# Performance work log

Hardware: AMD Instinct MI355X
Metric: run time of the kernel (lower is better)

The kernel has to match this reference:

```python
import jax, jax.numpy as jnp
import numpy as np

B, T, D, W, H = 4096, 1, 4096, 4, 512  # batch, step len, hidden, kernel_size, generator hidden


def setup_inputs() -> dict:
    key = jax.random.key(0)
    ks = jax.random.split(key, 5)
    x = jax.random.normal(ks[0], (B, T, D), dtype=jnp.float32)
    generator_input = jax.random.normal(ks[1], (B, T, D), dtype=jnp.float32)
    cache = jax.random.normal(ks[2], (B, D, W), dtype=jnp.float32)
    w1 = jax.random.normal(ks[3], (D, H), dtype=jnp.float32) * 0.02
    w2 = jax.random.normal(ks[4], (H, D * W), dtype=jnp.float32) * 0.02
    b2 = jnp.zeros((D * W,), dtype=jnp.float32)
    return {"x": x, "generator_input": generator_input, "cache": cache,
            "w1": w1, "w2": w2, "b2": b2}


def reference(x, generator_input, cache, w1, w2, b2):
    # --- kernel generator (DynamicShortConvolutionKernelGenerator) ---
    g = generator_input[:, 0]                        # [B, D]  (squeeze(1) in _step_triton)
    h = jax.nn.silu(g @ w1)                          # [B, H]
    flat_kernels = h @ w2 + b2                       # [B, D*W]
    kernels = flat_kernels.reshape(B, D, W)          # [B, D, W]  (rearrange 'b (d w) -> b d w')
    # --- causal_conv_step_triton: shift window left, append new token ---
    x_t = jnp.swapaxes(x, 1, 2)                      # [B, D, 1]
    new_cache = jnp.concatenate([cache[:, :, 1:], x_t], axis=-1)  # [B, D, W]
    # depthwise dynamic conv: per-token, per-channel kernel dot window
    out = jnp.sum(new_cache * kernels, axis=-1)      # [B, D]
    out = jax.nn.silu(out)[:, None, :]               # [B, 1, D] (view back to x shape)
    return out, new_cache
```

## Files before the change

kernel.cpp:

```cpp
#include <hip/hip_runtime.h>
#include <hip/hip_bf16.h>
#include <math.h>

#define B_  4096
#define D_  4096
#define W_  4
#define H_  512
#define NDW (D_*W_)

typedef float  f32x4  __attribute__((ext_vector_type(4)));
typedef __bf16 bf16x8 __attribute__((ext_vector_type(8)));

__device__ __forceinline__ unsigned short f32_to_bf16(float f) {
    unsigned int u = __float_as_uint(f);
    u += 0x7fffu + ((u >> 16) & 1u);
    return (unsigned short)(u >> 16);
}

__device__ __forceinline__ float silu_f(float v) {
    return v / (1.0f + __expf(-v));
}

__global__ void cast_g_kernel(const float* __restrict__ in,
                              unsigned short* __restrict__ out, int n4) {
    int i = blockIdx.x * blockDim.x + threadIdx.x;
    if (i >= n4) return;
    float4 v = ((const float4*)in)[i];
    ushort4 o;
    o.x = f32_to_bf16(v.x); o.y = f32_to_bf16(v.y);
    o.z = f32_to_bf16(v.z); o.w = f32_to_bf16(v.w);
    ((ushort4*)out)[i] = o;
}

__global__ void transpose_cast_kernel(const float* __restrict__ in,
                                      unsigned short* __restrict__ out,
                                      int R, int C) {
    __shared__ unsigned short tile[64][65];
    const int r0 = blockIdx.y * 64;
    const int c0 = blockIdx.x * 64;
    const int tx = threadIdx.x & 63;
    const int ty = threadIdx.x >> 6;
#pragma unroll
    for (int rr = ty; rr < 64; rr += 4)
        tile[rr][tx] = f32_to_bf16(in[(size_t)(r0 + rr) * C + c0 + tx]);
    __syncthreads();
#pragma unroll
    for (int cc = ty; cc < 64; cc += 4)
        out[(size_t)(c0 + cc) * R + r0 + tx] = tile[tx][cc];
}

template<int EPI>
__global__ __launch_bounds__(256)
void gemm_bt(const unsigned short* __restrict__ A,
             const unsigned short* __restrict__ Bt,
             unsigned short* __restrict__ Hout,
             float* __restrict__ Fout,
             const float* __restrict__ bias,
             int M, int N, int K)
{
    __shared__ unsigned short As[128 * 64];
    __shared__ unsigned short Bs[128 * 64];

    const int tid  = threadIdx.x;
    const int wave = tid >> 6;
    const int lane = tid & 63;
    const int quad = lane >> 4;
    const int l16  = lane & 15;
    const int m0 = blockIdx.y * 128;
    const int n0 = blockIdx.x * 128;
    const int wm = (wave >> 1) * 64;
    const int wn = (wave & 1) * 64;

    f32x4 acc[4][4];
#pragma unroll
    for (int i = 0; i < 4; ++i)
#pragma unroll
        for (int j = 0; j < 4; ++j)
            acc[i][j] = (f32x4){0.f, 0.f, 0.f, 0.f};

    for (int k0 = 0; k0 < K; k0 += 64) {
#pragma unroll
        for (int r = 0; r < 4; ++r) {
            const int flat  = r * 256 + tid;
            const int row   = flat >> 3;
            const int chunk = flat & 7;
            const unsigned short* gA = A  + (size_t)(m0 + row) * K + (k0 + chunk * 8);
            const unsigned short* gB = Bt + (size_t)(n0 + row) * K + (k0 + chunk * 8);
            unsigned short* lA = As + (size_t)(r * 256 + wave * 64) * 8;
            unsigned short* lB = Bs + (size_t)(r * 256 + wave * 64) * 8;
            __builtin_amdgcn_global_load_lds(
                (const __attribute__((address_space(1))) void*)gA,
                (__attribute__((address_space(3))) void*)lA, 16, 0, 0);
            __builtin_amdgcn_global_load_lds(
                (const __attribute__((address_space(1))) void*)gB,
                (__attribute__((address_space(3))) void*)lB, 16, 0, 0);
        }
        __syncthreads();

#pragma unroll
        for (int ks = 0; ks < 2; ++ks) {
            const int kk = ks * 32 + quad * 8;
            bf16x8 af[4], bfr[4];
#pragma unroll
            for (int i = 0; i < 4; ++i) {
                af[i]  = *(const bf16x8*)(As + (wm + i * 16 + l16) * 64 + kk);
                bfr[i] = *(const bf16x8*)(Bs + (wn + i * 16 + l16) * 64 + kk);
            }
#pragma unroll
            for (int i = 0; i < 4; ++i)
#pragma unroll
                for (int j = 0; j < 4; ++j)
                    acc[i][j] = __builtin_amdgcn_mfma_f32_16x16x32_bf16(
                        af[i], bfr[j], acc[i][j], 0, 0, 0);
        }
        __syncthreads();
    }

#pragma unroll
    for (int i = 0; i < 4; ++i) {
#pragma unroll
        for (int j = 0; j < 4; ++j) {
            const int col = n0 + wn + j * 16 + l16;
#pragma unroll
            for (int r = 0; r < 4; ++r) {
                const int row = m0 + wm + i * 16 + quad * 4 + r;
                float v = acc[i][j][r];
                if (EPI == 0) {
                    Hout[(size_t)row * N + col] = f32_to_bf16(silu_f(v));
                } else {
                    Fout[(size_t)row * N + col] = v + bias[col];
                }
            }
        }
    }
}

__global__ void conv_kernel(const float* __restrict__ x,
                            const float* __restrict__ cache,
                            float* __restrict__ out,
                            float* __restrict__ kc, int n) {
    int i = blockIdx.x * blockDim.x + threadIdx.x;
    if (i >= n) return;
    float4 k4 = ((const float4*)kc)[i];
    float4 c4 = ((const float4*)cache)[i];
    float  xv = x[i];
    float4 nc;
    nc.x = c4.y; nc.y = c4.z; nc.z = c4.w; nc.w = xv;
    float s = nc.x * k4.x + nc.y * k4.y + nc.z * k4.z + nc.w * k4.w;
    out[i] = silu_f(s);
    ((float4*)kc)[i] = nc;
}

extern "C" void kernel_launch(void* const* d_in, const int* in_sizes, int n_in,
                              void* d_out, int out_size, void* d_ws, size_t ws_size,
                              hipStream_t stream) {
    const float* x     = (const float*)d_in[0];
    const float* gin   = (const float*)d_in[1];
    const float* cache = (const float*)d_in[2];
    const float* w1    = (const float*)d_in[3];
    const float* w2    = (const float*)d_in[4];
    const float* b2    = (const float*)d_in[5];

    float* out    = (float*)d_out;
    float* ncache = out + (size_t)B_ * D_;

    unsigned short* g_bf = (unsigned short*)d_ws;
    unsigned short* w1t  = g_bf + (size_t)B_ * D_;
    unsigned short* w2t  = w1t + (size_t)H_ * D_;
    unsigned short* h_bf = w2t + (size_t)NDW * H_;

    cast_g_kernel<<<(B_ * D_ / 4 + 255) / 256, 256, 0, stream>>>(gin, g_bf, B_ * D_ / 4);
    transpose_cast_kernel<<<dim3(H_ / 64, D_ / 64), 256, 0, stream>>>(w1, w1t, D_, H_);
    transpose_cast_kernel<<<dim3(NDW / 64, H_ / 64), 256, 0, stream>>>(w2, w2t, H_, NDW);

    gemm_bt<0><<<dim3(H_ / 128, B_ / 128), 256, 0, stream>>>(
        g_bf, w1t, h_bf, nullptr, nullptr, B_, H_, D_);

    gemm_bt<1><<<dim3(NDW / 128, B_ / 128), 256, 0, stream>>>(
        h_bf, w2t, nullptr, ncache, b2, B_, NDW, H_);

    conv_kernel<<<(B_ * D_ + 255) / 256, 256, 0, stream>>>(x, cache, out, ncache, B_ * D_);
}
```

Measured before the change: 854.6 us.

## Fuse depthwise conv into second GEMM epilogue and shrink first GEMM M-tile

The second GEMM no longer writes the full B x D*W fp32 kernel tensor to global memory for a separate conv kernel to read back. It stages each half of its output tile in shared memory, adds the bias, and computes the shifted cache window, dot product, SiLU and new-cache write in place. The first GEMM now uses 64-row M tiles, doubling block count from 128 to 256 to fill more compute units. The cost is extra shared-memory staging, two additional barriers per block, and a longer epilogue.

```diff
diff --git a/kernel.cpp b/kernel.cpp
--- a/kernel.cpp
+++ b/kernel.cpp
@@ -49,17 +49,103 @@
         out[(size_t)(c0 + cc) * R + r0 + tx] = tile[tx][cc];
 }
 
-template<int EPI>
 __global__ __launch_bounds__(256)
-void gemm_bt(const unsigned short* __restrict__ A,
-             const unsigned short* __restrict__ Bt,
-             unsigned short* __restrict__ Hout,
-             float* __restrict__ Fout,
-             const float* __restrict__ bias,
-             int M, int N, int K)
+void gemm1_silu(const unsigned short* __restrict__ A,
+                const unsigned short* __restrict__ Bt,
+                unsigned short* __restrict__ Hout,
+                int M, int N, int K)
 {
-    __shared__ unsigned short As[128 * 64];
+    __shared__ unsigned short As[64 * 64];
     __shared__ unsigned short Bs[128 * 64];
+
+    const int tid  = threadIdx.x;
+    const int wave = tid >> 6;
+    const int lane = tid & 63;
+    const int quad = lane >> 4;
+    const int l16  = lane & 15;
+    const int m0 = blockIdx.y * 64;
+    const int n0 = blockIdx.x * 128;
+    const int wm = (wave >> 1) * 32;
+    const int wn = (wave & 1) * 64;
+
+    f32x4 acc[2][4];
+#pragma unroll
+    for (int i = 0; i < 2; ++i)
+#pragma unroll
+        for (int j = 0; j < 4; ++j)
+            acc[i][j] = (f32x4){0.f, 0.f, 0.f, 0.f};
+
+    for (int k0 = 0; k0 < K; k0 += 64) {
+#pragma unroll
+        for (int r = 0; r < 2; ++r) {
+            const int flat  = r * 256 + tid;
+            const int row   = flat >> 3;
+            const int chunk = flat & 7;
+            const unsigned short* gA = A + (size_t)(m0 + row) * K + (k0 + chunk * 8);
+            unsigned short* lA = As + (size_t)(r * 256 + wave * 64) * 8;
+            __builtin_amdgcn_global_load_lds(
+                (const __attribute__((address_space(1))) void*)gA,
+                (__attribute__((address_space(3))) void*)lA, 16, 0, 0);
+        }
+#pragma unroll
+        for (int r = 0; r < 4; ++r) {
+            const int flat  = r * 256 + tid;
+            const int row   = flat >> 3;
+            const int chunk = flat & 7;
+            const unsigned short* gB = Bt + (size_t)(n0 + row) * K + (k0 + chunk * 8);
+            unsigned short* lB = Bs + (size_t)(r * 256 + wave * 64) * 8;
+            __builtin_amdgcn_global_load_lds(
+                (const __attribute__((address_space(1))) void*)gB,
+                (__attribute__((address_space(3))) void*)lB, 16, 0, 0);
+        }
+        __syncthreads();
+
+#pragma unroll
+        for (int ks = 0; ks < 2; ++ks) {
+            const int kk = ks * 32 + quad * 8;
+            bf16x8 af[2], bfr[4];
+#pragma unroll
+            for (int i = 0; i < 2; ++i)
+                af[i]  = *(const bf16x8*)(As + (wm + i * 16 + l16) * 64 + kk);
+#pragma unroll
+            for (int j = 0; j < 4; ++j)
+                bfr[j] = *(const bf16x8*)(Bs + (wn + j * 16 + l16) * 64 + kk);
+#pragma unroll
+            for (int i = 0; i < 2; ++i)
+#pragma unroll
+                for (int j = 0; j < 4; ++j)
+                    acc[i][j] = __builtin_amdgcn_mfma_f32_16x16x32_bf16(
+                        af[i], bfr[j], acc[i][j], 0, 0, 0);
+        }
+        __syncthreads();
+    }
+
+#pragma unroll
+    for (int i = 0; i < 2; ++i)
+#pragma unroll
+        for (int j = 0; j < 4; ++j) {
+            const int col = n0 + wn + j * 16 + l16;
+#pragma unroll
+            for (int r = 0; r < 4; ++r) {
+                const int row = m0 + wm + i * 16 + quad * 4 + r;
+                Hout[(size_t)row * N + col] = f32_to_bf16(silu_f(acc[i][j][r]));
+            }
+        }
+}
+
+__global__ __launch_bounds__(256)
+void gemm2_conv(const unsigned short* __restrict__ A,
+                const unsigned short* __restrict__ Bt,
+                const float* __restrict__ bias,
+                const float* __restrict__ x,
+                const float* __restrict__ cache,
+                float* __restrict__ out,
+                float* __restrict__ ncache)
+{
+    __shared__ __align__(16) unsigned short smem[128 * 68 * 2];
+    unsigned short* As = smem;
+    unsigned short* Bs = smem + 128 * 64;
+    float* Cs = (float*)smem;
 
     const int tid  = threadIdx.x;
     const int wave = tid >> 6;
@@ -70,6 +156,7 @@
     const int n0 = blockIdx.x * 128;
     const int wm = (wave >> 1) * 64;
     const int wn = (wave & 1) * 64;
+    const int K = H_;
 
     f32x4 acc[4][4];
 #pragma unroll
@@ -117,38 +204,40 @@
     }
 
 #pragma unroll
-    for (int i = 0; i < 4; ++i) {
-#pragma unroll
-        for (int j = 0; j < 4; ++j) {
-            const int col = n0 + wn + j * 16 + l16;
-#pragma unroll
-            for (int r = 0; r < 4; ++r) {
-                const int row = m0 + wm + i * 16 + quad * 4 + r;
-                float v = acc[i][j][r];
-                if (EPI == 0) {
-                    Hout[(size_t)row * N + col] = f32_to_bf16(silu_f(v));
-                } else {
-                    Fout[(size_t)row * N + col] = v + bias[col];
+    for (int h = 0; h < 2; ++h) {
+        if ((wave & 1) == h) {
+#pragma unroll
+            for (int i = 0; i < 4; ++i)
+#pragma unroll
+                for (int j = 0; j < 4; ++j) {
+                    const int lc = j * 16 + l16;
+                    const float bv = bias[n0 + h * 64 + lc];
+#pragma unroll
+                    for (int r = 0; r < 4; ++r) {
+                        const int lr = wm + i * 16 + quad * 4 + r;
+                        Cs[lr * 68 + lc] = acc[i][j][r] + bv;
+                    }
                 }
-            }
-        }
+        }
+        __syncthreads();
+
+        const int dp    = tid & 15;
+        const int rbase = tid >> 4;
+        const int d     = (n0 >> 2) + h * 16 + dp;
+#pragma unroll
+        for (int rr = 0; rr < 8; ++rr) {
+            const int br = rr * 16 + rbase;
+            const size_t gi = (size_t)(m0 + br) * D_ + d;
+            f32x4 k4 = *(const f32x4*)(Cs + br * 68 + dp * 4);
+            f32x4 c4 = ((const f32x4*)cache)[gi];
+            float xv = x[gi];
+            f32x4 nc = { c4.y, c4.z, c4.w, xv };
+            float s = nc.x * k4.x + nc.y * k4.y + nc.z * k4.z + nc.w * k4.w;
+            out[gi] = silu_f(s);
+            ((f32x4*)ncache)[gi] = nc;
+        }
+        __syncthreads();
     }
-}
-
-__global__ void conv_kernel(const float* __restrict__ x,
-                            const float* __restrict__ cache,
-                            float* __restrict__ out,
-                            float* __restrict__ kc, int n) {
-    int i = blockIdx.x * blockDim.x + threadIdx.x;
-    if (i >= n) return;
-    float4 k4 = ((const float4*)kc)[i];
-    float4 c4 = ((const float4*)cache)[i];
-    float  xv = x[i];
-    float4 nc;
-    nc.x = c4.y; nc.y = c4.z; nc.z = c4.w; nc.w = xv;
-    float s = nc.x * k4.x + nc.y * k4.y + nc.z * k4.z + nc.w * k4.w;
-    out[i] = silu_f(s);
-    ((float4*)kc)[i] = nc;
 }
 
 extern "C" void kernel_launch(void* const* d_in, const int* in_sizes, int n_in,
@@ -173,11 +262,9 @@
     transpose_cast_kernel<<<dim3(H_ / 64, D_ / 64), 256, 0, stream>>>(w1, w1t, D_, H_);
     transpose_cast_kernel<<<dim3(NDW / 64, H_ / 64), 256, 0, stream>>>(w2, w2t, H_, NDW);
 
-    gemm_bt<0><<<dim3(H_ / 128, B_ / 128), 256, 0, stream>>>(
-        g_bf, w1t, h_bf, nullptr, nullptr, B_, H_, D_);
-
-    gemm_bt<1><<<dim3(NDW / 128, B_ / 128), 256, 0, stream>>>(
-        h_bf, w2t, nullptr, ncache, b2, B_, NDW, H_);
-
-    conv_kernel<<<(B_ * D_ + 255) / 256, 256, 0, stream>>>(x, cache, out, ncache, B_ * D_);
-}
+    gemm1_silu<<<dim3(H_ / 128, B_ / 64), 256, 0, stream>>>(
+        g_bf, w1t, h_bf, B_, H_, D_);
+
+    gemm2_conv<<<dim3(NDW / 128, B_ / 128), 256, 0, stream>>>(
+        h_bf, w2t, b2, x, cache, out, ncache);
+}
```

Result: faster. 777.7 us (-9.0%).
